# Kernel tuning notes

Hardware: AMD Instinct MI355X
Metric: run time of the kernel (lower is better)

## Reference

```python
import jax, jax.numpy as jnp
import numpy as np


def setup_inputs() -> dict:
    key = jax.random.key(0)
    bs, width, length = 4, 1536, 2048  # width = 3 * num_heads * ch = 3*8*64
    qkv = jax.random.normal(key, (bs, width, length), dtype=jnp.float32)
    return {"qkv": qkv, "num_heads": 8}


def reference(qkv, num_heads):
    bs, width, length = qkv.shape
    assert width % (3 * num_heads) == 0
    ch = width // (3 * num_heads)
    q, k, v = jnp.split(qkv, 3, axis=1)  # each [bs, num_heads*ch, length]
    scale = 1.0 / np.sqrt(np.sqrt(ch))  # applied to both q and k (total 1/sqrt(ch))
    q = (q * scale).reshape(bs * num_heads, ch, length)
    k = (k * scale).reshape(bs * num_heads, ch, length)
    v = v.reshape(bs * num_heads, ch, length)
    # weight[b, t, s] = sum_c q[b,c,t] * k[b,c,s]
    weight = jnp.einsum('bct,bcs->bts', q, k)
    weight = jax.nn.softmax(weight.astype(jnp.float32), axis=-1).astype(weight.dtype)
    # a[b, c, t] = sum_s weight[b,t,s] * v[b,c,s]
    a = jnp.einsum('bts,bcs->bct', weight, v)
    return a.reshape(bs, num_heads * ch, length)
```

## Files before the change

### kernel.cpp

```cpp
#include <hip/hip_runtime.h>

typedef float f32x16 __attribute__((ext_vector_type(16)));
typedef float f32x2 __attribute__((ext_vector_type(2)));
typedef short short8 __attribute__((ext_vector_type(8)));
typedef unsigned short u16;
typedef unsigned int u32;

#define SEQ_L 2048

#if __has_builtin(__builtin_amdgcn_exp2f)
#define EXP2(x) __builtin_amdgcn_exp2f(x)
#else
#define EXP2(x) exp2f(x)
#endif

__device__ __forceinline__ u32 pk2bf(float lo, float hi) {
#if __has_builtin(__builtin_amdgcn_cvt_pk_bf16_f32)
    typedef __bf16 bf16x2_t __attribute__((ext_vector_type(2)));
    union { bf16x2_t v; u32 i; } w;
    w.v = __builtin_amdgcn_cvt_pk_bf16_f32(lo, hi);
    return w.i;
#else
    union { float f; u32 i; } a, b; a.f = lo; b.f = hi;
    return ((a.i + 0x8000u) >> 16) | ((b.i + 0x8000u) & 0xFFFF0000u);
#endif
}

#define KT_U16 (64 * 64)
#define VT_STRIDE 72
#define VT_U16 (64 * VT_STRIDE)
#define GRP_U16 (KT_U16 + VT_U16)
#define BUF_U16 (2 * GRP_U16)
#define SMEM_U16 (2 * BUF_U16)

__global__ __launch_bounds__(512, 2)
void attn_kernel(const float* __restrict__ qkv, float* __restrict__ out) {
    const int tid  = threadIdx.x;
    const int lane = tid & 63;
    const int wv   = tid >> 6;
    const int g    = wv >> 2;
    const int wvin = wv & 3;
    const int col  = lane & 31;
    const int half = lane >> 5;

    const int gid  = blockIdx.x;
    const int head = gid & 31;
    const int tb   = gid >> 5;
    const int t0   = tb * 256 + wvin * 64;
    const int bb   = head >> 3, hh = head & 7;

    const size_t qoff = ((size_t)bb * 1536 + (size_t)hh * 64) * SEQ_L;
    const float* qp = qkv + qoff;
    const float* kp = qp + (size_t)512  * SEQ_L;
    const float* vp = qp + (size_t)1024 * SEQ_L;
    float* op = out + ((size_t)bb * 512 + (size_t)hh * 64) * SEQ_L;

    __shared__ __align__(16) u16 smem[SMEM_U16];
    u16* ktg = smem + g * GRP_U16;
    u16* vtg = ktg + KT_U16;

    const int gtid = tid & 255;
    const int sgrp = gtid & 15;
    const int rq   = gtid >> 4;
    const int sbase0 = g * 1024;

    u16* kw[4];
#pragma unroll
    for (int j = 0; j < 4; ++j) {
        int s = 4 * sgrp + j;
        int sw = ((s >> 2) ^ s) & 7;
        kw[j] = ktg + s * 64 + (((rq >> 1) ^ sw) << 3) + ((rq & 1) << 2);
    }
    const int vcoloff = ((sgrp >> 2) << 4) + ((sgrp & 1) << 3) + (((sgrp >> 1) & 1) << 2);
    u16* vw = vtg + rq * VT_STRIDE + vcoloff;

    const int sw_r = ((col >> 2) ^ col) & 7;
    int kco[4];
#pragma unroll
    for (int ks = 0; ks < 4; ++ks) kco[ks] = ((2 * ks + half) ^ sw_r) << 3;
    const u16* krb0 = ktg + col * 64;
    const u16* krb1 = ktg + (32 + col) * 64;
    const u16* vrb0 = vtg + col * VT_STRIDE + half * 8;
    const u16* vrb1 = vtg + (32 + col) * VT_STRIDE + half * 8;

    const int tA = t0 + col;
    const int tB = tA + 32;
    const float qscale = 0.18033688f;
    short8 qfA[4], qfB[4];
#pragma unroll
    for (int ks = 0; ks < 4; ++ks) {
        union { u32 u[4]; short8 v; } qa, qb;
#pragma unroll
        for (int e2 = 0; e2 < 4; ++e2) {
            int c = ks * 16 + half * 8 + 2 * e2;
            const float* c0 = qp + (size_t)c * SEQ_L;
            const float* c1 = qp + (size_t)(c + 1) * SEQ_L;
            qa.u[e2] = pk2bf(c0[tA] * qscale, c1[tA] * qscale);
            qb.u[e2] = pk2bf(c0[tB] * qscale, c1[tB] * qscale);
        }
        qfA[ks] = qa.v; qfB[ks] = qb.v;
    }

    f32x16 zacc;
#pragma unroll
    for (int r = 0; r < 16; ++r) zacc[r] = 0.0f;

    f32x16 accO[2][2];
#pragma unroll
    for (int tt = 0; tt < 2; ++tt)
#pragma unroll
        for (int m = 0; m < 2; ++m)
#pragma unroll
            for (int r = 0; r < 16; ++r) accO[tt][m][r] = 0.0f;
    f32x2 lsA = {0.0f, 0.0f}, lsB = {0.0f, 0.0f};

    float4 kreg[4], vreg[4];
    auto load_tile = [&](int itt) {
        const int sn = sbase0 + itt * 64;
#pragma unroll
        for (int rr = 0; rr < 4; ++rr) {
            kreg[rr] = *(const float4*)(kp + (size_t)(4 * rq + rr) * SEQ_L + sn + 4 * sgrp);
            vreg[rr] = *(const float4*)(vp + (size_t)(rq + 16 * rr) * SEQ_L + sn + 4 * sgrp);
        }
    };
    auto publish = [&](int bo) {
#pragma unroll
        for (int j = 0; j < 4; ++j) {
            uint2 w;
            w.x = pk2bf(kreg[0][j], kreg[1][j]);
            w.y = pk2bf(kreg[2][j], kreg[3][j]);
            *(uint2*)(kw[j] + bo) = w;
        }
#pragma unroll
        for (int rr = 0; rr < 4; ++rr) {
            uint2 w;
            w.x = pk2bf(vreg[rr].x, vreg[rr].y);
            w.y = pk2bf(vreg[rr].z, vreg[rr].w);
            *(uint2*)(vw + bo + 16 * rr * VT_STRIDE) = w;
        }
    };

    load_tile(0);
    publish(0);
    load_tile(1);

#pragma unroll 2
    for (int it = 0; it < 16; ++it) {
        __syncthreads();
        const int bo_c = (it & 1) * BUF_U16;
        const int bo_n = ((it + 1) & 1) * BUF_U16;

        if (it + 1 < 16) publish(bo_n);
        if (it + 2 < 16) load_tile(it + 2);

        f32x16 accA[2], accB[2];
        __builtin_amdgcn_s_setprio(1);
#pragma unroll
        for (int mb = 0; mb < 2; ++mb) {
            const u16* rb = (mb ? krb1 : krb0) + bo_c;
            short8 kf0 = *(const short8*)(rb + kco[0]);
            accA[mb] = __builtin_amdgcn_mfma_f32_32x32x16_bf16(kf0, qfA[0], zacc, 0, 0, 0);
            accB[mb] = __builtin_amdgcn_mfma_f32_32x32x16_bf16(kf0, qfB[0], zacc, 0, 0, 0);
#pragma unroll
            for (int ks = 1; ks < 4; ++ks) {
                short8 kf = *(const short8*)(rb + kco[ks]);
                accA[mb] = __builtin_amdgcn_mfma_f32_32x32x16_bf16(kf, qfA[ks], accA[mb], 0, 0, 0);
                accB[mb] = __builtin_amdgcn_mfma_f32_32x32x16_bf16(kf, qfB[ks], accB[mb], 0, 0, 0);
            }
        }
        __builtin_amdgcn_s_setprio(0);

        u32 pregA[2][8], pregB[2][8];
#pragma unroll
        for (int mb = 0; mb < 2; ++mb) {
            f32x2 a2[4], b2[4];
#pragma unroll
            for (int u2 = 0; u2 < 8; ++u2) {
                float ax = EXP2(accA[mb][2 * u2]);
                float ay = EXP2(accA[mb][2 * u2 + 1]);
                pregA[mb][u2] = pk2bf(ax, ay);
                f32x2 av = {ax, ay};
                if (u2 < 4) a2[u2] = av; else a2[u2 - 4] += av;
            }
            lsA += (a2[0] + a2[1]) + (a2[2] + a2[3]);
#pragma unroll
            for (int u2 = 0; u2 < 8; ++u2) {
                float bx = EXP2(accB[mb][2 * u2]);
                float by = EXP2(accB[mb][2 * u2 + 1]);
                pregB[mb][u2] = pk2bf(bx, by);
                f32x2 bv = {bx, by};
                if (u2 < 4) b2[u2] = bv; else b2[u2 - 4] += bv;
            }
            lsB += (b2[0] + b2[1]) + (b2[2] + b2[3]);
        }

        __builtin_amdgcn_s_setprio(1);
#pragma unroll
        for (int mk = 0; mk < 4; ++mk) {
            int mb = mk >> 1, kb = mk & 1;
            union { u32 u[4]; short8 v; } bfA, bfB;
#pragma unroll
            for (int i = 0; i < 4; ++i) {
                bfA.u[i] = pregA[mb][4 * kb + i];
                bfB.u[i] = pregB[mb][4 * kb + i];
            }
#pragma unroll
            for (int mbc = 0; mbc < 2; ++mbc) {
                short8 vf = *(const short8*)((mbc ? vrb1 : vrb0) + bo_c + mk * 16);
                accO[0][mbc] = __builtin_amdgcn_mfma_f32_32x32x16_bf16(vf, bfA.v, accO[0][mbc], 0, 0, 0);
                accO[1][mbc] = __builtin_amdgcn_mfma_f32_32x32x16_bf16(vf, bfB.v, accO[1][mbc], 0, 0, 0);
            }
        }
        __builtin_amdgcn_s_setprio(0);
    }

    float lsum[2];
    lsum[0] = lsA[0] + lsA[1];
    lsum[1] = lsB[0] + lsB[1];

    __syncthreads();
    float* ep = (float*)smem;
    if (g == 1) {
#pragma unroll
        for (int tt = 0; tt < 2; ++tt) {
            float* row = ep + ((wvin * 64 + lane) * 2 + tt) * 33;
#pragma unroll
            for (int mbc = 0; mbc < 2; ++mbc)
#pragma unroll
                for (int r = 0; r < 16; ++r) row[mbc * 16 + r] = accO[tt][mbc][r];
            row[32] = lsum[tt];
        }
    }
    __syncthreads();
    if (g == 0) {
#pragma unroll
        for (int tt = 0; tt < 2; ++tt) {
            const float* row = ep + ((wvin * 64 + lane) * 2 + tt) * 33;
#pragma unroll
            for (int mbc = 0; mbc < 2; ++mbc)
#pragma unroll
                for (int r = 0; r < 16; ++r) accO[tt][mbc][r] += row[mbc * 16 + r];
            float lt = lsum[tt] + row[32];
            float ltot = lt + __shfl_xor(lt, 32, 64);
            float inv = 1.0f / ltot;
            const int t = tt ? tB : tA;
#pragma unroll
            for (int mbc = 0; mbc < 2; ++mbc) {
#pragma unroll
                for (int r = 0; r < 16; ++r) {
                    int c = mbc * 32 + (r & 3) + 8 * (r >> 2) + 4 * half;
                    op[(size_t)c * SEQ_L + t] = accO[tt][mbc][r] * inv;
                }
            }
        }
    }
}

extern "C" void kernel_launch(void* const* d_in, const int* in_sizes, int n_in,
                              void* d_out, int out_size, void* d_ws, size_t ws_size,
                              hipStream_t stream) {
    (void)in_sizes; (void)n_in; (void)d_ws; (void)ws_size; (void)out_size;
    const float* qkv = (const float*)d_in[0];
    float* out = (float*)d_out;
    attn_kernel<<<dim3(256), dim3(512), 0, stream>>>(qkv, out);
}
```

Baseline: 121.9 us.

## Interleave exp of B tile with PV MFMAs of A tile, prefetch LDS fragments

Reorders the per-iteration loop body. K fragments are loaded from LDS into registers up front. The global load for tile it+2 is moved after the QK MFMAs. The softmax exp of the second query tile now runs after the first tile's PV MFMAs, so VALU exp work can overlap with matrix-core work. V fragments are loaded once and reused for both tiles. Keeping more fragments live raises register pressure, which may cut occupancy or cause spills.

```diff
diff --git a/kernel.cpp b/kernel.cpp
--- a/kernel.cpp
+++ b/kernel.cpp
@@ -150,30 +150,37 @@
         const int bo_c = (it & 1) * BUF_U16;
         const int bo_n = ((it + 1) & 1) * BUF_U16;
 
+        short8 kfr[2][4];
+#pragma unroll
+        for (int mb = 0; mb < 2; ++mb) {
+            const u16* rb = (mb ? krb1 : krb0) + bo_c;
+#pragma unroll
+            for (int ks = 0; ks < 4; ++ks)
+                kfr[mb][ks] = *(const short8*)(rb + kco[ks]);
+        }
+
         if (it + 1 < 16) publish(bo_n);
-        if (it + 2 < 16) load_tile(it + 2);
 
         f32x16 accA[2], accB[2];
         __builtin_amdgcn_s_setprio(1);
 #pragma unroll
         for (int mb = 0; mb < 2; ++mb) {
-            const u16* rb = (mb ? krb1 : krb0) + bo_c;
-            short8 kf0 = *(const short8*)(rb + kco[0]);
-            accA[mb] = __builtin_amdgcn_mfma_f32_32x32x16_bf16(kf0, qfA[0], zacc, 0, 0, 0);
-            accB[mb] = __builtin_amdgcn_mfma_f32_32x32x16_bf16(kf0, qfB[0], zacc, 0, 0, 0);
+            accA[mb] = __builtin_amdgcn_mfma_f32_32x32x16_bf16(kfr[mb][0], qfA[0], zacc, 0, 0, 0);
+            accB[mb] = __builtin_amdgcn_mfma_f32_32x32x16_bf16(kfr[mb][0], qfB[0], zacc, 0, 0, 0);
 #pragma unroll
             for (int ks = 1; ks < 4; ++ks) {
-                short8 kf = *(const short8*)(rb + kco[ks]);
-                accA[mb] = __builtin_amdgcn_mfma_f32_32x32x16_bf16(kf, qfA[ks], accA[mb], 0, 0, 0);
-                accB[mb] = __builtin_amdgcn_mfma_f32_32x32x16_bf16(kf, qfB[ks], accB[mb], 0, 0, 0);
+                accA[mb] = __builtin_amdgcn_mfma_f32_32x32x16_bf16(kfr[mb][ks], qfA[ks], accA[mb], 0, 0, 0);
+                accB[mb] = __builtin_amdgcn_mfma_f32_32x32x16_bf16(kfr[mb][ks], qfB[ks], accB[mb], 0, 0, 0);
             }
         }
         __builtin_amdgcn_s_setprio(0);
 
-        u32 pregA[2][8], pregB[2][8];
-#pragma unroll
-        for (int mb = 0; mb < 2; ++mb) {
-            f32x2 a2[4], b2[4];
+        if (it + 2 < 16) load_tile(it + 2);
+
+        u32 pregA[2][8];
+#pragma unroll
+        for (int mb = 0; mb < 2; ++mb) {
+            f32x2 a2[4];
 #pragma unroll
             for (int u2 = 0; u2 < 8; ++u2) {
                 float ax = EXP2(accA[mb][2 * u2]);
@@ -183,6 +190,32 @@
                 if (u2 < 4) a2[u2] = av; else a2[u2 - 4] += av;
             }
             lsA += (a2[0] + a2[1]) + (a2[2] + a2[3]);
+        }
+
+        short8 vfr[2][4];
+#pragma unroll
+        for (int mbc = 0; mbc < 2; ++mbc)
+#pragma unroll
+            for (int mk = 0; mk < 4; ++mk)
+                vfr[mbc][mk] = *(const short8*)((mbc ? vrb1 : vrb0) + bo_c + mk * 16);
+
+        __builtin_amdgcn_s_setprio(1);
+#pragma unroll
+        for (int mk = 0; mk < 4; ++mk) {
+            int mb = mk >> 1, kb = mk & 1;
+            union { u32 u[4]; short8 v; } bfA;
+#pragma unroll
+            for (int i = 0; i < 4; ++i) bfA.u[i] = pregA[mb][4 * kb + i];
+#pragma unroll
+            for (int mbc = 0; mbc < 2; ++mbc)
+                accO[0][mbc] = __builtin_amdgcn_mfma_f32_32x32x16_bf16(vfr[mbc][mk], bfA.v, accO[0][mbc], 0, 0, 0);
+        }
+        __builtin_amdgcn_s_setprio(0);
+
+        u32 pregB[2][8];
+#pragma unroll
+        for (int mb = 0; mb < 2; ++mb) {
+            f32x2 b2[4];
 #pragma unroll
             for (int u2 = 0; u2 < 8; ++u2) {
                 float bx = EXP2(accB[mb][2 * u2]);
@@ -198,18 +231,12 @@
 #pragma unroll
         for (int mk = 0; mk < 4; ++mk) {
             int mb = mk >> 1, kb = mk & 1;
-            union { u32 u[4]; short8 v; } bfA, bfB;
-#pragma unroll
-            for (int i = 0; i < 4; ++i) {
-                bfA.u[i] = pregA[mb][4 * kb + i];
-                bfB.u[i] = pregB[mb][4 * kb + i];
-            }
-#pragma unroll
-            for (int mbc = 0; mbc < 2; ++mbc) {
-                short8 vf = *(const short8*)((mbc ? vrb1 : vrb0) + bo_c + mk * 16);
-                accO[0][mbc] = __builtin_amdgcn_mfma_f32_32x32x16_bf16(vf, bfA.v, accO[0][mbc], 0, 0, 0);
-                accO[1][mbc] = __builtin_amdgcn_mfma_f32_32x32x16_bf16(vf, bfB.v, accO[1][mbc], 0, 0, 0);
-            }
+            union { u32 u[4]; short8 v; } bfB;
+#pragma unroll
+            for (int i = 0; i < 4; ++i) bfB.u[i] = pregB[mb][4 * kb + i];
+#pragma unroll
+            for (int mbc = 0; mbc < 2; ++mbc)
+                accO[1][mbc] = __builtin_amdgcn_mfma_f32_32x32x16_bf16(vfr[mbc][mk], bfB.v, accO[1][mbc], 0, 0, 0);
         }
         __builtin_amdgcn_s_setprio(0);
     }
```

Measured after the change: 221.1 us. 81.5% more time.

## Halve query rows per wave and double grid to raise CU occupancy

Applied to the files above, without the earlier changes.

Each wave now computes 32 query positions instead of 64, so a block covers 128 queries and the grid doubles to 512 blocks. The second accumulator set (B-tile MFMAs, exps and output accumulators) is dropped, and launch bounds now request 4 blocks per CU. The aim is to fill the GPU with more concurrent waves and cut per-thread register pressure. In exchange, each K/V tile load and LDS publish now feeds half as many MFMAs, which doubles global K/V traffic. The 4-blocks-per-CU register limit may also force spills, while LDS size probably caps residency at fewer blocks anyway.

```diff
diff --git a/kernel.cpp b/kernel.cpp
--- a/kernel.cpp
+++ b/kernel.cpp
@@ -33,7 +33,7 @@
 #define BUF_U16 (2 * GRP_U16)
 #define SMEM_U16 (2 * BUF_U16)
 
-__global__ __launch_bounds__(512, 2)
+__global__ __launch_bounds__(512, 4)
 void attn_kernel(const float* __restrict__ qkv, float* __restrict__ out) {
     const int tid  = threadIdx.x;
     const int lane = tid & 63;
@@ -46,7 +46,7 @@
     const int gid  = blockIdx.x;
     const int head = gid & 31;
     const int tb   = gid >> 5;
-    const int t0   = tb * 256 + wvin * 64;
+    const int t0   = tb * 128 + wvin * 32;
     const int bb   = head >> 3, hh = head & 7;
 
     const size_t qoff = ((size_t)bb * 1536 + (size_t)hh * 64) * SEQ_L;
@@ -84,35 +84,31 @@
     const u16* vrb1 = vtg + (32 + col) * VT_STRIDE + half * 8;
 
     const int tA = t0 + col;
-    const int tB = tA + 32;
     const float qscale = 0.18033688f;
-    short8 qfA[4], qfB[4];
+    short8 qfA[4];
 #pragma unroll
     for (int ks = 0; ks < 4; ++ks) {
-        union { u32 u[4]; short8 v; } qa, qb;
+        union { u32 u[4]; short8 v; } qa;
 #pragma unroll
         for (int e2 = 0; e2 < 4; ++e2) {
             int c = ks * 16 + half * 8 + 2 * e2;
             const float* c0 = qp + (size_t)c * SEQ_L;
             const float* c1 = qp + (size_t)(c + 1) * SEQ_L;
             qa.u[e2] = pk2bf(c0[tA] * qscale, c1[tA] * qscale);
-            qb.u[e2] = pk2bf(c0[tB] * qscale, c1[tB] * qscale);
-        }
-        qfA[ks] = qa.v; qfB[ks] = qb.v;
+        }
+        qfA[ks] = qa.v;
     }
 
     f32x16 zacc;
 #pragma unroll
     for (int r = 0; r < 16; ++r) zacc[r] = 0.0f;
 
-    f32x16 accO[2][2];
-#pragma unroll
-    for (int tt = 0; tt < 2; ++tt)
-#pragma unroll
-        for (int m = 0; m < 2; ++m)
-#pragma unroll
-            for (int r = 0; r < 16; ++r) accO[tt][m][r] = 0.0f;
-    f32x2 lsA = {0.0f, 0.0f}, lsB = {0.0f, 0.0f};
+    f32x16 accO[2];
+#pragma unroll
+    for (int m = 0; m < 2; ++m)
+#pragma unroll
+        for (int r = 0; r < 16; ++r) accO[m][r] = 0.0f;
+    f32x2 lsA = {0.0f, 0.0f};
 
     float4 kreg[4], vreg[4];
     auto load_tile = [&](int itt) {
@@ -153,27 +149,25 @@
         if (it + 1 < 16) publish(bo_n);
         if (it + 2 < 16) load_tile(it + 2);
 
-        f32x16 accA[2], accB[2];
+        f32x16 accA[2];
         __builtin_amdgcn_s_setprio(1);
 #pragma unroll
         for (int mb = 0; mb < 2; ++mb) {
             const u16* rb = (mb ? krb1 : krb0) + bo_c;
             short8 kf0 = *(const short8*)(rb + kco[0]);
             accA[mb] = __builtin_amdgcn_mfma_f32_32x32x16_bf16(kf0, qfA[0], zacc, 0, 0, 0);
-            accB[mb] = __builtin_amdgcn_mfma_f32_32x32x16_bf16(kf0, qfB[0], zacc, 0, 0, 0);
 #pragma unroll
             for (int ks = 1; ks < 4; ++ks) {
                 short8 kf = *(const short8*)(rb + kco[ks]);
                 accA[mb] = __builtin_amdgcn_mfma_f32_32x32x16_bf16(kf, qfA[ks], accA[mb], 0, 0, 0);
-                accB[mb] = __builtin_amdgcn_mfma_f32_32x32x16_bf16(kf, qfB[ks], accB[mb], 0, 0, 0);
             }
         }
         __builtin_amdgcn_s_setprio(0);
 
-        u32 pregA[2][8], pregB[2][8];
+        u32 pregA[2][8];
 #pragma unroll
         for (int mb = 0; mb < 2; ++mb) {
-            f32x2 a2[4], b2[4];
+            f32x2 a2[4];
 #pragma unroll
             for (int u2 = 0; u2 < 8; ++u2) {
                 float ax = EXP2(accA[mb][2 * u2]);
@@ -183,74 +177,52 @@
                 if (u2 < 4) a2[u2] = av; else a2[u2 - 4] += av;
             }
             lsA += (a2[0] + a2[1]) + (a2[2] + a2[3]);
-#pragma unroll
-            for (int u2 = 0; u2 < 8; ++u2) {
-                float bx = EXP2(accB[mb][2 * u2]);
-                float by = EXP2(accB[mb][2 * u2 + 1]);
-                pregB[mb][u2] = pk2bf(bx, by);
-                f32x2 bv = {bx, by};
-                if (u2 < 4) b2[u2] = bv; else b2[u2 - 4] += bv;
-            }
-            lsB += (b2[0] + b2[1]) + (b2[2] + b2[3]);
         }
 
         __builtin_amdgcn_s_setprio(1);
 #pragma unroll
         for (int mk = 0; mk < 4; ++mk) {
             int mb = mk >> 1, kb = mk & 1;
-            union { u32 u[4]; short8 v; } bfA, bfB;
-#pragma unroll
-            for (int i = 0; i < 4; ++i) {
-                bfA.u[i] = pregA[mb][4 * kb + i];
-                bfB.u[i] = pregB[mb][4 * kb + i];
-            }
+            union { u32 u[4]; short8 v; } bfA;
+#pragma unroll
+            for (int i = 0; i < 4; ++i) bfA.u[i] = pregA[mb][4 * kb + i];
 #pragma unroll
             for (int mbc = 0; mbc < 2; ++mbc) {
                 short8 vf = *(const short8*)((mbc ? vrb1 : vrb0) + bo_c + mk * 16);
-                accO[0][mbc] = __builtin_amdgcn_mfma_f32_32x32x16_bf16(vf, bfA.v, accO[0][mbc], 0, 0, 0);
-                accO[1][mbc] = __builtin_amdgcn_mfma_f32_32x32x16_bf16(vf, bfB.v, accO[1][mbc], 0, 0, 0);
+                accO[mbc] = __builtin_amdgcn_mfma_f32_32x32x16_bf16(vf, bfA.v, accO[mbc], 0, 0, 0);
             }
         }
         __builtin_amdgcn_s_setprio(0);
     }
 
-    float lsum[2];
-    lsum[0] = lsA[0] + lsA[1];
-    lsum[1] = lsB[0] + lsB[1];
+    float lsum = lsA[0] + lsA[1];
 
     __syncthreads();
     float* ep = (float*)smem;
     if (g == 1) {
-#pragma unroll
-        for (int tt = 0; tt < 2; ++tt) {
-            float* row = ep + ((wvin * 64 + lane) * 2 + tt) * 33;
-#pragma unroll
-            for (int mbc = 0; mbc < 2; ++mbc)
-#pragma unroll
-                for (int r = 0; r < 16; ++r) row[mbc * 16 + r] = accO[tt][mbc][r];
-            row[32] = lsum[tt];
-        }
+        float* row = ep + (wvin * 64 + lane) * 33;
+#pragma unroll
+        for (int mbc = 0; mbc < 2; ++mbc)
+#pragma unroll
+            for (int r = 0; r < 16; ++r) row[mbc * 16 + r] = accO[mbc][r];
+        row[32] = lsum;
     }
     __syncthreads();
     if (g == 0) {
-#pragma unroll
-        for (int tt = 0; tt < 2; ++tt) {
-            const float* row = ep + ((wvin * 64 + lane) * 2 + tt) * 33;
-#pragma unroll
-            for (int mbc = 0; mbc < 2; ++mbc)
-#pragma unroll
-                for (int r = 0; r < 16; ++r) accO[tt][mbc][r] += row[mbc * 16 + r];
-            float lt = lsum[tt] + row[32];
-            float ltot = lt + __shfl_xor(lt, 32, 64);
-            float inv = 1.0f / ltot;
-            const int t = tt ? tB : tA;
-#pragma unroll
-            for (int mbc = 0; mbc < 2; ++mbc) {
-#pragma unroll
-                for (int r = 0; r < 16; ++r) {
-                    int c = mbc * 32 + (r & 3) + 8 * (r >> 2) + 4 * half;
-                    op[(size_t)c * SEQ_L + t] = accO[tt][mbc][r] * inv;
-                }
+        const float* row = ep + (wvin * 64 + lane) * 33;
+#pragma unroll
+        for (int mbc = 0; mbc < 2; ++mbc)
+#pragma unroll
+            for (int r = 0; r < 16; ++r) accO[mbc][r] += row[mbc * 16 + r];
+        float lt = lsum + row[32];
+        float ltot = lt + __shfl_xor(lt, 32, 64);
+        float inv = 1.0f / ltot;
+#pragma unroll
+        for (int mbc = 0; mbc < 2; ++mbc) {
+#pragma unroll
+            for (int r = 0; r < 16; ++r) {
+                int c = mbc * 32 + (r & 3) + 8 * (r >> 2) + 4 * half;
+                op[(size_t)c * SEQ_L + tA] = accO[mbc][r] * inv;
             }
         }
     }
@@ -262,5 +234,5 @@
     (void)in_sizes; (void)n_in; (void)d_ws; (void)ws_size; (void)out_size;
     const float* qkv = (const float*)d_in[0];
     float* out = (float*)d_out;
-    attn_kernel<<<dim3(256), dim3(512), 0, stream>>>(qkv, out);
+    attn_kernel<<<dim3(512), dim3(512), 0, stream>>>(qkv, out);
 }
```

Measured after the change: 193.9 us. 1.59x slower.
